# Optimization experiments

Hardware: AMD Instinct MI355X
Metric: run time of the kernel (lower is better)

## Reference

```python
import jax, jax.numpy as jnp
import numpy as np

B, T, D = 4096, 256, 64          # batch, steps, state_dim
LD, CD = 4, 8                    # latent_dim, categorical_dim
H = 32                           # mlp_hidden
FEAT = D + LD * CD               # fc1 input dim


def setup_inputs() -> dict:
    key = jax.random.key(0)
    ks = jax.random.split(key, 8)
    states = jax.random.normal(ks[0], (B, T, D), dtype=jnp.float32)
    # pre-sampled Gumbel(0,1) noise, as used inside F.gumbel_softmax
    u = jax.random.uniform(ks[1], (B, T, LD, CD), jnp.float32, 1e-6, 1.0 - 1e-6)
    gumbel = -jnp.log(-jnp.log(u))
    tau = jnp.float32(1.0)
    def lin(k, fan_in, fan_out):
        bound = 1.0 / np.sqrt(fan_in)
        kw, kb = jax.random.split(k)
        W = jax.random.uniform(kw, (fan_in, fan_out), jnp.float32, -bound, bound)
        b = jax.random.uniform(kb, (fan_out,), jnp.float32, -bound, bound)
        return W, b
    W1, b1 = lin(ks[2], FEAT, H)
    W2, b2 = lin(ks[3], H, H)
    W3, b3 = lin(ks[4], H, LD * CD)
    return {"states": states, "gumbel": gumbel, "tau": tau,
            "W1": W1, "b1": b1, "W2": W2, "b2": b2, "W3": W3, "b3": b3}


def reference(states, gumbel, tau, W1, b1, W2, b2, W3, b3):
    Bs, T, _ = states.shape
    ld, cd = gumbel.shape[2], gumbel.shape[3]
    # init_states: eye(cd)[0] tiled latent_dim times -> [B, ld*cd]
    c0 = jnp.tile(jax.nn.one_hot(0, cd, dtype=states.dtype), (Bs, ld))
    xs = (jnp.swapaxes(states, 0, 1), jnp.swapaxes(gumbel, 0, 1))  # [T,B,...]

    def step(c, x):
        s, g = x                                   # s:[B,D], g:[B,ld,cd]
        z = jnp.concatenate([s, c], axis=-1)       # [B, FEAT]
        h1 = jax.nn.relu(z @ W1 + b1)
        h2 = jax.nn.relu(h1 @ W2 + b2)
        q = (h2 @ W3 + b3).reshape(Bs, ld, cd)
        y_soft = jax.nn.softmax((q + g) / tau, axis=-1)
        # hard=True (eval mode) straight-through one-hot
        y_hard = jax.nn.one_hot(jnp.argmax(y_soft, axis=-1), cd, dtype=y_soft.dtype)
        y = y_hard + y_soft - jax.lax.stop_gradient(y_soft)
        c_new = y.reshape(Bs, ld * cd)
        return c_new, c_new

    _, out = jax.lax.scan(step, c0, xs)            # [T, B, ld*cd]
    return jnp.swapaxes(out, 0, 1)                 # [B, T, ld*cd]
```

## Files before the change

kernel.cpp:

```cpp
#include <hip/hip_runtime.h>

#define NB   4096
#define NT   256
#define ND   64

template <int CTRL>
__device__ __forceinline__ float dppf(float x) {
  return __int_as_float(__builtin_amdgcn_update_dpp(
      0, __float_as_int(x), CTRL, 0xF, 0xF, false));
}
#define ROR16(x) dppf<0x121>(x)
__device__ __forceinline__ float max8(float x) {
  float t = fmaxf(x, dppf<0xB1>(x));
  t = fmaxf(t, dppf<0x4E>(t));
  t = fmaxf(t, dppf<0x141>(t));
  return t;
}

#define ROTMAC(WA, WB, WC, WD)                          \
  _Pragma("unroll")                                     \
  for (int r = 0; r < 16; ++r) {                        \
    a0 = fmaf(vl, WA[r], a0);                           \
    a1 = fmaf(vh, WB[r], a1);                           \
    a2 = fmaf(vl, WC[r], a2);                           \
    a3 = fmaf(vh, WD[r], a3);                           \
    if (r < 15) { vl = ROR16(vl); vh = ROR16(vh); }     \
  }

__global__ __launch_bounds__(256)
void h1pre_kernel(const float* __restrict__ S,
                  const float* __restrict__ W1,
                  const float* __restrict__ b1,
                  float* __restrict__ out) {
  const int row = blockIdx.x * 256 + threadIdx.x;
  const float4* srow = (const float4*)(S + (size_t)row * ND);

  float acc[32];
#pragma unroll
  for (int j = 0; j < 32; ++j) acc[j] = b1[j];

#pragma unroll
  for (int kc = 0; kc < 4; ++kc) {
    float4 x[4];
#pragma unroll
    for (int i = 0; i < 4; ++i) x[i] = srow[kc * 4 + i];
#pragma unroll
    for (int i = 0; i < 4; ++i) {
      const float xv[4] = {x[i].x, x[i].y, x[i].z, x[i].w};
#pragma unroll
      for (int kk = 0; kk < 4; ++kk) {
        const int k = kc * 16 + i * 4 + kk;
        const float xk = xv[kk];
#pragma unroll
        for (int j = 0; j < 32; ++j)
          acc[j] = fmaf(xk, W1[k * 32 + j], acc[j]);
      }
    }
  }

  float4* orow = (float4*)(out + (size_t)row * 32);
#pragma unroll
  for (int j4 = 0; j4 < 8; ++j4)
    orow[j4] = make_float4(acc[4 * j4], acc[4 * j4 + 1],
                           acc[4 * j4 + 2], acc[4 * j4 + 3]);
}

__global__ __launch_bounds__(256, 1)
void rec_kernel(const float* __restrict__ G,
                const float* __restrict__ W1,
                const float* __restrict__ W2,
                const float* __restrict__ b2,
                const float* __restrict__ W3,
                const float* __restrict__ b3,
                float* __restrict__ out) {
  const int tid  = threadIdx.x;
  const int wave = tid >> 6;
  const int lane = tid & 63;
  const int bw   = lane >> 4;
  const int s    = lane & 15;
  const int b    = blockIdx.x * 16 + wave * 4 + bw;

  float w1A[16], w1B[16], w1C[16], w1D[16];
  float w2A[16], w2B[16], w2C[16], w2D[16];
  float w3A[16], w3B[16], w3C[16], w3D[16];
#pragma unroll
  for (int r = 0; r < 16; ++r) {
    const int klo = (s - r) & 15;
    const int khi = klo + 16;
    w1A[r] = W1[(64 + klo) * 32 + s];
    w1B[r] = W1[(64 + khi) * 32 + s];
    w1C[r] = W1[(64 + klo) * 32 + s + 16];
    w1D[r] = W1[(64 + khi) * 32 + s + 16];
    w2A[r] = W2[klo * 32 + s];
    w2B[r] = W2[khi * 32 + s];
    w2C[r] = W2[klo * 32 + s + 16];
    w2D[r] = W2[khi * 32 + s + 16];
    w3A[r] = W3[klo * 32 + s];
    w3B[r] = W3[khi * 32 + s];
    w3C[r] = W3[klo * 32 + s + 16];
    w3D[r] = W3[khi * 32 + s + 16];
  }
  const float b2l = b2[s], b2h = b2[s + 16];
  const float b3l = b3[s], b3h = b3[s + 16];

  float clo = (s == 0 || s == 8) ? 1.f : 0.f;
  float chi = clo;

  const size_t gbase = ((size_t)b * NT) * 32 + s;
  const size_t obase = ((size_t)b * NT) * 32 + s;
  float gA0 = G[gbase + 0 * 32], gA1 = G[gbase + 0 * 32 + 16];
  float gB0 = G[gbase + 1 * 32], gB1 = G[gbase + 1 * 32 + 16];
  float hA0 = out[obase + 0 * 32], hA1 = out[obase + 0 * 32 + 16];
  float hB0 = out[obase + 1 * 32], hB1 = out[obase + 1 * 32 + 16];

#pragma unroll 1
  for (int t = 0; t < NT; ++t) {
    const int tp = (t + 2 < NT) ? t + 2 : NT - 1;
    const float hC0 = out[obase + (size_t)tp * 32];
    const float hC1 = out[obase + (size_t)tp * 32 + 16];
    const float gC0 = G[gbase + (size_t)tp * 32];
    const float gC1 = G[gbase + (size_t)tp * 32 + 16];

    float a0 = hA0, a1 = 0.f, a2 = hA1, a3 = 0.f;
    float vl = clo, vh = chi;
    ROTMAC(w1A, w1B, w1C, w1D)
    float hl = fmaxf(a0 + a1, 0.f);
    float hh = fmaxf(a2 + a3, 0.f);

    a0 = b2l; a1 = 0.f; a2 = b2h; a3 = 0.f; vl = hl; vh = hh;
    ROTMAC(w2A, w2B, w2C, w2D)
    hl = fmaxf(a0 + a1, 0.f);
    hh = fmaxf(a2 + a3, 0.f);

    a0 = b3l + gA0; a1 = 0.f; a2 = b3h + gA1; a3 = 0.f; vl = hl; vh = hh;
    ROTMAC(w3A, w3B, w3C, w3D)
    const float q0 = a0 + a1;
    const float q1 = a2 + a3;

    const float m0 = max8(q0);
    const float m1 = max8(q1);
    const unsigned long long bl0 = __ballot(q0 == m0);
    const unsigned long long bl1 = __ballot(q1 == m1);
    const int sh = lane & 56;
    const unsigned gr0 = (unsigned)(bl0 >> sh) & 255u;
    const unsigned gr1 = (unsigned)(bl1 >> sh) & 255u;
    const int my = lane & 7;
    const float y0 = ((__ffs(gr0) - 1) == my) ? 1.f : 0.f;
    const float y1 = ((__ffs(gr1) - 1) == my) ? 1.f : 0.f;

    out[obase + (size_t)t * 32]      = y0;
    out[obase + (size_t)t * 32 + 16] = y1;

    clo = y0; chi = y1;
    hA0 = hB0; hA1 = hB1; hB0 = hC0; hB1 = hC1;
    gA0 = gB0; gA1 = gB1; gB0 = gC0; gB1 = gC1;
  }
}

extern "C" void kernel_launch(void* const* d_in, const int* in_sizes, int n_in,
                              void* d_out, int out_size, void* d_ws, size_t ws_size,
                              hipStream_t stream) {
  const float* S  = (const float*)d_in[0];
  const float* G  = (const float*)d_in[1];
  const float* W1 = (const float*)d_in[3];
  const float* b1 = (const float*)d_in[4];
  const float* W2 = (const float*)d_in[5];
  const float* b2 = (const float*)d_in[6];
  const float* W3 = (const float*)d_in[7];
  const float* b3 = (const float*)d_in[8];
  float* out = (float*)d_out;

  hipLaunchKernelGGL(h1pre_kernel, dim3((NB * NT) / 256), dim3(256), 0, stream,
                     S, W1, b1, out);
  hipLaunchKernelGGL(rec_kernel, dim3(NB / 16), dim3(256), 0, stream,
                     G, W1, W2, b2, W3, b3, out);
}
```

Baseline: 777.1 us.

## Remap recurrent kernel to 32 lanes per batch row with direct DPP rotations

After: 764.5 us. Within noise of the previous version (-1.6%).

```diff
diff --git a/kernel.cpp b/kernel.cpp
--- a/kernel.cpp
+++ b/kernel.cpp
@@ -5,11 +5,18 @@
 #define ND   64
 
 template <int CTRL>
+__device__ __forceinline__ float rotr(float x) {
+  return __int_as_float(__builtin_amdgcn_update_dpp(
+      0, __float_as_int(x), CTRL, 0xF, 0xF, true));
+}
+__device__ __forceinline__ float swz16(float x) {
+  return __int_as_float(__builtin_amdgcn_ds_swizzle(__float_as_int(x), 0x401F));
+}
+template <int CTRL>
 __device__ __forceinline__ float dppf(float x) {
   return __int_as_float(__builtin_amdgcn_update_dpp(
-      0, __float_as_int(x), CTRL, 0xF, 0xF, false));
+      0, __float_as_int(x), CTRL, 0xF, 0xF, true));
 }
-#define ROR16(x) dppf<0x121>(x)
 __device__ __forceinline__ float max8(float x) {
   float t = fmaxf(x, dppf<0xB1>(x));
   t = fmaxf(t, dppf<0x4E>(t));
@@ -17,14 +24,29 @@
   return t;
 }
 
-#define ROTMAC(WA, WB, WC, WD)                          \
-  _Pragma("unroll")                                     \
-  for (int r = 0; r < 16; ++r) {                        \
-    a0 = fmaf(vl, WA[r], a0);                           \
-    a1 = fmaf(vh, WB[r], a1);                           \
-    a2 = fmaf(vl, WC[r], a2);                           \
-    a3 = fmaf(vh, WD[r], a3);                           \
-    if (r < 15) { vl = ROR16(vl); vh = ROR16(vh); }     \
+#define RSTEP(r, acc, v, w) acc = fmaf(rotr<0x120 + r>(v), w[r], acc)
+
+#define LAYER16(vA, vB, wA, wB, initA, q)                  \
+  {                                                        \
+    float a0 = (initA), a1 = 0.f, c0 = 0.f, c1 = 0.f;      \
+    a0 = fmaf((vA), wA[0], a0);                            \
+    c0 = fmaf((vB), wB[0], c0);                            \
+    RSTEP(1, a1, vA, wA);  RSTEP(1, c1, vB, wB);           \
+    RSTEP(2, a0, vA, wA);  RSTEP(2, c0, vB, wB);           \
+    RSTEP(3, a1, vA, wA);  RSTEP(3, c1, vB, wB);           \
+    RSTEP(4, a0, vA, wA);  RSTEP(4, c0, vB, wB);           \
+    RSTEP(5, a1, vA, wA);  RSTEP(5, c1, vB, wB);           \
+    RSTEP(6, a0, vA, wA);  RSTEP(6, c0, vB, wB);           \
+    RSTEP(7, a1, vA, wA);  RSTEP(7, c1, vB, wB);           \
+    RSTEP(8, a0, vA, wA);  RSTEP(8, c0, vB, wB);           \
+    RSTEP(9, a1, vA, wA);  RSTEP(9, c1, vB, wB);           \
+    RSTEP(10, a0, vA, wA); RSTEP(10, c0, vB, wB);          \
+    RSTEP(11, a1, vA, wA); RSTEP(11, c1, vB, wB);          \
+    RSTEP(12, a0, vA, wA); RSTEP(12, c0, vB, wB);          \
+    RSTEP(13, a1, vA, wA); RSTEP(13, c1, vB, wB);          \
+    RSTEP(14, a0, vA, wA); RSTEP(14, c0, vB, wB);          \
+    RSTEP(15, a1, vA, wA); RSTEP(15, c1, vB, wB);          \
+    q = (a0 + a1) + (c0 + c1);                             \
   }
 
 __global__ __launch_bounds__(256)
@@ -32,40 +54,46 @@
                   const float* __restrict__ W1,
                   const float* __restrict__ b1,
                   float* __restrict__ out) {
-  const int row = blockIdx.x * 256 + threadIdx.x;
-  const float4* srow = (const float4*)(S + (size_t)row * ND);
+  const size_t pid = (size_t)blockIdx.x * 256 + threadIdx.x;
+  const float4* s0 = (const float4*)(S + pid * 2 * ND);
+  const float4* s1 = s0 + (ND / 4);
 
-  float acc[32];
+  float acc0[32], acc1[32];
 #pragma unroll
-  for (int j = 0; j < 32; ++j) acc[j] = b1[j];
+  for (int j = 0; j < 32; ++j) { acc0[j] = b1[j]; acc1[j] = b1[j]; }
 
 #pragma unroll
   for (int kc = 0; kc < 4; ++kc) {
-    float4 x[4];
+    float4 x0[4], x1[4];
 #pragma unroll
-    for (int i = 0; i < 4; ++i) x[i] = srow[kc * 4 + i];
+    for (int i = 0; i < 4; ++i) { x0[i] = s0[kc * 4 + i]; x1[i] = s1[kc * 4 + i]; }
 #pragma unroll
     for (int i = 0; i < 4; ++i) {
-      const float xv[4] = {x[i].x, x[i].y, x[i].z, x[i].w};
+      const float v0[4] = {x0[i].x, x0[i].y, x0[i].z, x0[i].w};
+      const float v1[4] = {x1[i].x, x1[i].y, x1[i].z, x1[i].w};
 #pragma unroll
       for (int kk = 0; kk < 4; ++kk) {
         const int k = kc * 16 + i * 4 + kk;
-        const float xk = xv[kk];
 #pragma unroll
-        for (int j = 0; j < 32; ++j)
-          acc[j] = fmaf(xk, W1[k * 32 + j], acc[j]);
+        for (int j = 0; j < 32; ++j) {
+          const float w = W1[k * 32 + j];
+          acc0[j] = fmaf(v0[kk], w, acc0[j]);
+          acc1[j] = fmaf(v1[kk], w, acc1[j]);
+        }
       }
     }
   }
 
-  float4* orow = (float4*)(out + (size_t)row * 32);
+  float4* o0 = (float4*)(out + pid * 2 * 32);
+  float4* o1 = o0 + 8;
 #pragma unroll
-  for (int j4 = 0; j4 < 8; ++j4)
-    orow[j4] = make_float4(acc[4 * j4], acc[4 * j4 + 1],
-                           acc[4 * j4 + 2], acc[4 * j4 + 3]);
+  for (int q = 0; q < 8; ++q) {
+    o0[q] = make_float4(acc0[4*q], acc0[4*q+1], acc0[4*q+2], acc0[4*q+3]);
+    o1[q] = make_float4(acc1[4*q], acc1[4*q+1], acc1[4*q+2], acc1[4*q+3]);
+  }
 }
 
-__global__ __launch_bounds__(256, 1)
+__global__ __launch_bounds__(256, 2)
 void rec_kernel(const float* __restrict__ G,
                 const float* __restrict__ W1,
                 const float* __restrict__ W2,
@@ -76,84 +104,58 @@
   const int tid  = threadIdx.x;
   const int wave = tid >> 6;
   const int lane = tid & 63;
-  const int bw   = lane >> 4;
   const int s    = lane & 15;
-  const int b    = blockIdx.x * 16 + wave * 4 + bw;
+  const int half = (lane >> 4) & 1;
+  const int j    = s + 16 * half;
+  const int b    = blockIdx.x * 8 + wave * 2 + (lane >> 5);
 
-  float w1A[16], w1B[16], w1C[16], w1D[16];
-  float w2A[16], w2B[16], w2C[16], w2D[16];
-  float w3A[16], w3B[16], w3C[16], w3D[16];
+  float w1A[16], w1B[16], w2A[16], w2B[16], w3A[16], w3B[16];
 #pragma unroll
   for (int r = 0; r < 16; ++r) {
-    const int klo = (s - r) & 15;
-    const int khi = klo + 16;
-    w1A[r] = W1[(64 + klo) * 32 + s];
-    w1B[r] = W1[(64 + khi) * 32 + s];
-    w1C[r] = W1[(64 + klo) * 32 + s + 16];
-    w1D[r] = W1[(64 + khi) * 32 + s + 16];
-    w2A[r] = W2[klo * 32 + s];
-    w2B[r] = W2[khi * 32 + s];
-    w2C[r] = W2[klo * 32 + s + 16];
-    w2D[r] = W2[khi * 32 + s + 16];
-    w3A[r] = W3[klo * 32 + s];
-    w3B[r] = W3[khi * 32 + s];
-    w3C[r] = W3[klo * 32 + s + 16];
-    w3D[r] = W3[khi * 32 + s + 16];
+    const int kA = ((s - r) & 15) + 16 * half;
+    const int kB = ((s - r) & 15) + 16 * (1 - half);
+    w1A[r] = W1[(64 + kA) * 32 + j];
+    w1B[r] = W1[(64 + kB) * 32 + j];
+    w2A[r] = W2[kA * 32 + j];
+    w2B[r] = W2[kB * 32 + j];
+    w3A[r] = W3[kA * 32 + j];
+    w3B[r] = W3[kB * 32 + j];
   }
-  const float b2l = b2[s], b2h = b2[s + 16];
-  const float b3l = b3[s], b3h = b3[s + 16];
+  const float b2j = b2[j];
+  const float b3j = b3[j];
 
-  float clo = (s == 0 || s == 8) ? 1.f : 0.f;
-  float chi = clo;
+  float vA = (s % 8 == 0) ? 1.f : 0.f;
+  float vB = vA;
 
-  const size_t gbase = ((size_t)b * NT) * 32 + s;
-  const size_t obase = ((size_t)b * NT) * 32 + s;
-  float gA0 = G[gbase + 0 * 32], gA1 = G[gbase + 0 * 32 + 16];
-  float gB0 = G[gbase + 1 * 32], gB1 = G[gbase + 1 * 32 + 16];
-  float hA0 = out[obase + 0 * 32], hA1 = out[obase + 0 * 32 + 16];
-  float hB0 = out[obase + 1 * 32], hB1 = out[obase + 1 * 32 + 16];
+  const size_t base = ((size_t)b * NT) * 32 + j;
+  float gA = G[base], gB = G[base + 32];
+  float hA = out[base], hB = out[base + 32];
 
 #pragma unroll 1
   for (int t = 0; t < NT; ++t) {
     const int tp = (t + 2 < NT) ? t + 2 : NT - 1;
-    const float hC0 = out[obase + (size_t)tp * 32];
-    const float hC1 = out[obase + (size_t)tp * 32 + 16];
-    const float gC0 = G[gbase + (size_t)tp * 32];
-    const float gC1 = G[gbase + (size_t)tp * 32 + 16];
+    const float gC = G[base + (size_t)tp * 32];
+    const float hC = out[base + (size_t)tp * 32];
 
-    float a0 = hA0, a1 = 0.f, a2 = hA1, a3 = 0.f;
-    float vl = clo, vh = chi;
-    ROTMAC(w1A, w1B, w1C, w1D)
-    float hl = fmaxf(a0 + a1, 0.f);
-    float hh = fmaxf(a2 + a3, 0.f);
+    float q;
+    LAYER16(vA, vB, w1A, w1B, hA, q);
+    float tq = swz16(q);
+    float xA = fmaxf(q, 0.f), xB = fmaxf(tq, 0.f);
+    LAYER16(xA, xB, w2A, w2B, b2j, q);
+    tq = swz16(q);
+    xA = fmaxf(q, 0.f); xB = fmaxf(tq, 0.f);
+    LAYER16(xA, xB, w3A, w3B, b3j + gA, q);
 
-    a0 = b2l; a1 = 0.f; a2 = b2h; a3 = 0.f; vl = hl; vh = hh;
-    ROTMAC(w2A, w2B, w2C, w2D)
-    hl = fmaxf(a0 + a1, 0.f);
-    hh = fmaxf(a2 + a3, 0.f);
+    const float m = max8(q);
+    const unsigned long long bl = __ballot(q == m);
+    const unsigned gr = (unsigned)(bl >> (lane & 56)) & 255u;
+    const float y = ((__ffs(gr) - 1) == (lane & 7)) ? 1.f : 0.f;
 
-    a0 = b3l + gA0; a1 = 0.f; a2 = b3h + gA1; a3 = 0.f; vl = hl; vh = hh;
-    ROTMAC(w3A, w3B, w3C, w3D)
-    const float q0 = a0 + a1;
-    const float q1 = a2 + a3;
+    out[base + (size_t)t * 32] = y;
 
-    const float m0 = max8(q0);
-    const float m1 = max8(q1);
-    const unsigned long long bl0 = __ballot(q0 == m0);
-    const unsigned long long bl1 = __ballot(q1 == m1);
-    const int sh = lane & 56;
-    const unsigned gr0 = (unsigned)(bl0 >> sh) & 255u;
-    const unsigned gr1 = (unsigned)(bl1 >> sh) & 255u;
-    const int my = lane & 7;
-    const float y0 = ((__ffs(gr0) - 1) == my) ? 1.f : 0.f;
-    const float y1 = ((__ffs(gr1) - 1) == my) ? 1.f : 0.f;
-
-    out[obase + (size_t)t * 32]      = y0;
-    out[obase + (size_t)t * 32 + 16] = y1;
-
-    clo = y0; chi = y1;
-    hA0 = hB0; hA1 = hB1; hB0 = hC0; hB1 = hC1;
-    gA0 = gB0; gA1 = gB1; gB0 = gC0; gB1 = gC1;
+    vA = y;
+    vB = swz16(y);
+    hA = hB; hB = hC; gA = gB; gB = gC;
   }
 }
 
@@ -170,8 +172,8 @@
   const float* b3 = (const float*)d_in[8];
   float* out = (float*)d_out;
 
-  hipLaunchKernelGGL(h1pre_kernel, dim3((NB * NT) / 256), dim3(256), 0, stream,
+  hipLaunchKernelGGL(h1pre_kernel, dim3((NB * NT / 2) / 256), dim3(256), 0, stream,
                      S, W1, b1, out);
-  hipLaunchKernelGGL(rec_kernel, dim3(NB / 16), dim3(256), 0, stream,
+  hipLaunchKernelGGL(rec_kernel, dim3(NB / 8), dim3(256), 0, stream,
                      G, W1, W2, b2, W3, b3, out);
 }
```

## Spread each batch row across a full wave with split-K and bpermute reductions

Applied to the files above, without the earlier changes.

Measured after the change: 751.8 us. -3.3%, faster.

```diff
diff --git a/kernel.cpp b/kernel.cpp
--- a/kernel.cpp
+++ b/kernel.cpp
@@ -7,9 +7,11 @@
 template <int CTRL>
 __device__ __forceinline__ float dppf(float x) {
   return __int_as_float(__builtin_amdgcn_update_dpp(
-      0, __float_as_int(x), CTRL, 0xF, 0xF, false));
+      0, __float_as_int(x), CTRL, 0xF, 0xF, true));
 }
-#define ROR16(x) dppf<0x121>(x)
+__device__ __forceinline__ float bperm(int addr, float x) {
+  return __int_as_float(__builtin_amdgcn_ds_bpermute(addr, __float_as_int(x)));
+}
 __device__ __forceinline__ float max8(float x) {
   float t = fmaxf(x, dppf<0xB1>(x));
   t = fmaxf(t, dppf<0x4E>(t));
@@ -17,29 +19,39 @@
   return t;
 }
 
-#define ROTMAC(WA, WB, WC, WD)                          \
-  _Pragma("unroll")                                     \
-  for (int r = 0; r < 16; ++r) {                        \
-    a0 = fmaf(vl, WA[r], a0);                           \
-    a1 = fmaf(vh, WB[r], a1);                           \
-    a2 = fmaf(vl, WC[r], a2);                           \
-    a3 = fmaf(vh, WD[r], a3);                           \
-    if (r < 15) { vl = ROR16(vl); vh = ROR16(vh); }     \
-  }
+__device__ __forceinline__ float mac16(float v, const float w[16], float init) {
+  float a0 = fmaf(v, w[0], init);
+  float a1 = dppf<0x121>(v) * w[1];
+  a0 = fmaf(dppf<0x122>(v), w[2], a0);
+  a1 = fmaf(dppf<0x123>(v), w[3], a1);
+  a0 = fmaf(dppf<0x124>(v), w[4], a0);
+  a1 = fmaf(dppf<0x125>(v), w[5], a1);
+  a0 = fmaf(dppf<0x126>(v), w[6], a0);
+  a1 = fmaf(dppf<0x127>(v), w[7], a1);
+  a0 = fmaf(dppf<0x128>(v), w[8], a0);
+  a1 = fmaf(dppf<0x129>(v), w[9], a1);
+  a0 = fmaf(dppf<0x12A>(v), w[10], a0);
+  a1 = fmaf(dppf<0x12B>(v), w[11], a1);
+  a0 = fmaf(dppf<0x12C>(v), w[12], a0);
+  a1 = fmaf(dppf<0x12D>(v), w[13], a1);
+  a0 = fmaf(dppf<0x12E>(v), w[14], a0);
+  a1 = fmaf(dppf<0x12F>(v), w[15], a1);
+  return a0 + a1;
+}
 
 __global__ __launch_bounds__(256)
 void h1pre_kernel(const float* __restrict__ S,
                   const float* __restrict__ W1,
                   const float* __restrict__ b1,
                   float* __restrict__ out) {
-  const int row = blockIdx.x * 256 + threadIdx.x;
-  const float4* srow = (const float4*)(S + (size_t)row * ND);
+  const size_t row = (size_t)blockIdx.x * 256 + threadIdx.x;
+  const float4* srow = (const float4*)(S + row * ND);
 
   float acc[32];
 #pragma unroll
   for (int j = 0; j < 32; ++j) acc[j] = b1[j];
 
-#pragma unroll
+#pragma unroll 1
   for (int kc = 0; kc < 4; ++kc) {
     float4 x[4];
 #pragma unroll
@@ -50,22 +62,20 @@
 #pragma unroll
       for (int kk = 0; kk < 4; ++kk) {
         const int k = kc * 16 + i * 4 + kk;
-        const float xk = xv[kk];
 #pragma unroll
         for (int j = 0; j < 32; ++j)
-          acc[j] = fmaf(xk, W1[k * 32 + j], acc[j]);
+          acc[j] = fmaf(xv[kk], W1[k * 32 + j], acc[j]);
       }
     }
   }
 
-  float4* orow = (float4*)(out + (size_t)row * 32);
+  float4* orow = (float4*)(out + row * 32);
 #pragma unroll
-  for (int j4 = 0; j4 < 8; ++j4)
-    orow[j4] = make_float4(acc[4 * j4], acc[4 * j4 + 1],
-                           acc[4 * j4 + 2], acc[4 * j4 + 3]);
+  for (int q = 0; q < 8; ++q)
+    orow[q] = make_float4(acc[4*q], acc[4*q+1], acc[4*q+2], acc[4*q+3]);
 }
 
-__global__ __launch_bounds__(256, 1)
+__global__ __launch_bounds__(256, 4)
 void rec_kernel(const float* __restrict__ G,
                 const float* __restrict__ W1,
                 const float* __restrict__ W2,
@@ -76,84 +86,64 @@
   const int tid  = threadIdx.x;
   const int wave = tid >> 6;
   const int lane = tid & 63;
-  const int bw   = lane >> 4;
   const int s    = lane & 15;
-  const int b    = blockIdx.x * 16 + wave * 4 + bw;
+  const int g    = lane >> 4;
+  const int jh   = g & 1;
+  const int kh   = g >> 1;
+  const int j    = s + 16 * jh;
+  const int b    = blockIdx.x * 4 + wave;
+  const bool lo  = (lane < 32);
 
-  float w1A[16], w1B[16], w1C[16], w1D[16];
-  float w2A[16], w2B[16], w2C[16], w2D[16];
-  float w3A[16], w3B[16], w3C[16], w3D[16];
+  float w1[16], w2[16], w3[16];
 #pragma unroll
   for (int r = 0; r < 16; ++r) {
-    const int klo = (s - r) & 15;
-    const int khi = klo + 16;
-    w1A[r] = W1[(64 + klo) * 32 + s];
-    w1B[r] = W1[(64 + khi) * 32 + s];
-    w1C[r] = W1[(64 + klo) * 32 + s + 16];
-    w1D[r] = W1[(64 + khi) * 32 + s + 16];
-    w2A[r] = W2[klo * 32 + s];
-    w2B[r] = W2[khi * 32 + s];
-    w2C[r] = W2[klo * 32 + s + 16];
-    w2D[r] = W2[khi * 32 + s + 16];
-    w3A[r] = W3[klo * 32 + s];
-    w3B[r] = W3[khi * 32 + s];
-    w3C[r] = W3[klo * 32 + s + 16];
-    w3D[r] = W3[khi * 32 + s + 16];
+    const int k = ((s - r) & 15) + 16 * kh;
+    w1[r] = W1[(64 + k) * 32 + j];
+    w2[r] = W2[k * 32 + j];
+    w3[r] = W3[k * 32 + j];
   }
-  const float b2l = b2[s], b2h = b2[s + 16];
-  const float b3l = b3[s], b3h = b3[s + 16];
+  const float bias2 = lo ? b2[j] : 0.f;
+  const float bias3 = lo ? b3[j] : 0.f;
 
-  float clo = (s == 0 || s == 8) ? 1.f : 0.f;
-  float chi = clo;
+  const int a_x32 = (lane ^ 32) << 2;
+  const int a_rd  = (s + 16 * kh) << 2;
 
-  const size_t gbase = ((size_t)b * NT) * 32 + s;
-  const size_t obase = ((size_t)b * NT) * 32 + s;
-  float gA0 = G[gbase + 0 * 32], gA1 = G[gbase + 0 * 32 + 16];
-  float gB0 = G[gbase + 1 * 32], gB1 = G[gbase + 1 * 32 + 16];
-  float hA0 = out[obase + 0 * 32], hA1 = out[obase + 0 * 32 + 16];
-  float hB0 = out[obase + 1 * 32], hB1 = out[obase + 1 * 32 + 16];
+  float v = (s % 8 == 0) ? 1.f : 0.f;
+
+  const size_t base = ((size_t)b * NT) * 32 + (lane & 31);
+  float hA = out[base], hB = out[base + 32];
+  float gA = G[base],   gB = G[base + 32];
+
+  const int sh = lane & 56;
+  const int my = lane & 7;
 
 #pragma unroll 1
   for (int t = 0; t < NT; ++t) {
     const int tp = (t + 2 < NT) ? t + 2 : NT - 1;
-    const float hC0 = out[obase + (size_t)tp * 32];
-    const float hC1 = out[obase + (size_t)tp * 32 + 16];
-    const float gC0 = G[gbase + (size_t)tp * 32];
-    const float gC1 = G[gbase + (size_t)tp * 32 + 16];
+    const float hC = out[base + (size_t)tp * 32];
+    const float gC = G[base + (size_t)tp * 32];
 
-    float a0 = hA0, a1 = 0.f, a2 = hA1, a3 = 0.f;
-    float vl = clo, vh = chi;
-    ROTMAC(w1A, w1B, w1C, w1D)
-    float hl = fmaxf(a0 + a1, 0.f);
-    float hh = fmaxf(a2 + a3, 0.f);
+    const float p1 = mac16(v, w1, lo ? hA : 0.f);
+    float q = p1 + bperm(a_x32, p1);
+    v = bperm(a_rd, fmaxf(q, 0.f));
 
-    a0 = b2l; a1 = 0.f; a2 = b2h; a3 = 0.f; vl = hl; vh = hh;
-    ROTMAC(w2A, w2B, w2C, w2D)
-    hl = fmaxf(a0 + a1, 0.f);
-    hh = fmaxf(a2 + a3, 0.f);
+    const float p2 = mac16(v, w2, bias2);
+    q = p2 + bperm(a_x32, p2);
+    v = bperm(a_rd, fmaxf(q, 0.f));
 
-    a0 = b3l + gA0; a1 = 0.f; a2 = b3h + gA1; a3 = 0.f; vl = hl; vh = hh;
-    ROTMAC(w3A, w3B, w3C, w3D)
-    const float q0 = a0 + a1;
-    const float q1 = a2 + a3;
+    const float p3 = mac16(v, w3, lo ? (bias3 + gA) : 0.f);
+    q = p3 + bperm(a_x32, p3);
 
-    const float m0 = max8(q0);
-    const float m1 = max8(q1);
-    const unsigned long long bl0 = __ballot(q0 == m0);
-    const unsigned long long bl1 = __ballot(q1 == m1);
-    const int sh = lane & 56;
-    const unsigned gr0 = (unsigned)(bl0 >> sh) & 255u;
-    const unsigned gr1 = (unsigned)(bl1 >> sh) & 255u;
-    const int my = lane & 7;
-    const float y0 = ((__ffs(gr0) - 1) == my) ? 1.f : 0.f;
-    const float y1 = ((__ffs(gr1) - 1) == my) ? 1.f : 0.f;
+    const float m = max8(q);
+    const unsigned long long bl = __ballot(q == m);
+    const unsigned gr = (unsigned)(bl >> sh) & 255u;
+    const float y = ((__ffs(gr) - 1) == my) ? 1.f : 0.f;
 
-    out[obase + (size_t)t * 32]      = y0;
-    out[obase + (size_t)t * 32 + 16] = y1;
+    if (lo) out[base + (size_t)t * 32] = y;
 
-    clo = y0; chi = y1;
-    hA0 = hB0; hA1 = hB1; hB0 = hC0; hB1 = hC1;
-    gA0 = gB0; gA1 = gB1; gB0 = gC0; gB1 = gC1;
+    v = bperm(a_rd, y);
+
+    hA = hB; hB = hC; gA = gB; gB = gC;
   }
 }
 
@@ -172,6 +162,6 @@
 
   hipLaunchKernelGGL(h1pre_kernel, dim3((NB * NT) / 256), dim3(256), 0, stream,
                      S, W1, b1, out);
-  hipLaunchKernelGGL(rec_kernel, dim3(NB / 16), dim3(256), 0, stream,
+  hipLaunchKernelGGL(rec_kernel, dim3(NB / 4), dim3(256), 0, stream,
                      G, W1, W2, b2, W3, b3, out);
 }
```
